# Optimization experiments

Hardware: AMD Instinct MI355X
Metric: run time of the kernel (lower is better)

## Reference

```python
import jax, jax.numpy as jnp
import numpy as np

BETA = 0.9
TH = 1.0
SLOPE = 25.0  # fast-sigmoid surrogate slope (spike_grad_slope)

@jax.custom_vjp
def spike_fn(m):
    # Heaviside on (mem - threshold)
    return (m > 0).astype(m.dtype)

def _spike_fwd(m):
    return spike_fn(m), m

def _spike_bwd(m, g):
    # fast-sigmoid surrogate gradient: 1 / (slope*|m| + 1)^2
    return (g / (SLOPE * jnp.abs(m) + 1.0) ** 2,)

spike_fn.defvjp(_spike_fwd, _spike_bwd)


def setup_inputs() -> dict:
    key = jax.random.key(0)
    k1, k2, k3 = jax.random.split(key, 3)
    T, B, I, H, O = 128, 8192, 2, 256, 2
    x = jax.random.normal(k1, (T, B, I), dtype=jnp.float32)
    # xavier_uniform with gain=1: limit = sqrt(6/(fan_in+fan_out))
    lim1 = float(np.sqrt(6.0 / (I + H)))
    lim2 = float(np.sqrt(6.0 / (H + O)))
    W1 = jax.random.uniform(k2, (H, I), jnp.float32, -lim1, lim1)
    W2 = jax.random.uniform(k3, (O, H), jnp.float32, -lim2, lim2)
    return {"x": x, "W1": W1, "W2": W2}


def reference(x, W1, W2):
    # Precompute all per-step input currents in one GEMM: [T,B,H]
    cur = jnp.einsum('tbi,hi->tbh', x, W1)
    B, H = cur.shape[1], cur.shape[2]
    mem0 = jnp.zeros((B, H), cur.dtype)

    def step(mem, c):
        # snntorch Leaky (reset_mechanism='subtract'):
        # reset based on PREVIOUS mem's spike, then leaky integrate, then fire
        reset = spike_fn(mem - TH)
        mem_new = BETA * mem + c - reset * TH
        spk = spike_fn(mem_new - TH)
        # original code detaches mem between steps (1-step truncated BPTT)
        return jax.lax.stop_gradient(mem_new), spk

    _, spk_rec = jax.lax.scan(step, mem0, cur)  # spk_rec: [T,B,H]
    spk_avg = spk_rec[-10:].mean(0)             # [B,H]
    out = jnp.einsum('bh,oh->bo', spk_avg, W2)  # [B,O]
    return out
```

## Files before the change

### kernel.cpp

```cpp
#include <hip/hip_runtime.h>


#define T_STEPS 128
#define BATCH   8192
#define HID     256
#define TAIL    10
#define RH      8
#define NP      (RH/2)
#define LB      64
#define NWAVE   4
#define HG      8
#define NBG     (BATCH / LB)
#define PF      8

typedef float f32x2 __attribute__((ext_vector_type(2)));

#define PK_MUL(d, a, b) asm("v_pk_mul_f32 %0, %1, %2" : "=v"(d) : "v"(a), "v"(b))
#define PK_ADD(d, a, b) asm("v_pk_add_f32 %0, %1, %2" : "=v"(d) : "v"(a), "v"(b))

__device__ unsigned int bg_done[NBG];

__global__ __launch_bounds__(256) void snn_scan(const float* __restrict__ x,
                                                const float* __restrict__ W1,
                                                const float* __restrict__ W2,
                                                float2* __restrict__ partial,
                                                float2* __restrict__ out) {
    const int tid   = threadIdx.x;
    const int lane  = tid & 63;
    const int wave  = tid >> 6;
    const int bg    = blockIdx.x & (NBG - 1);
    const int hg    = blockIdx.x >> 7;
    const int b     = bg * LB + lane;
    const int hbase = hg * (NWAVE * RH) + wave * RH;

    f32x2 w01[RH];
    const f32x2* w1v = (const f32x2*)W1;
#pragma unroll
    for (int r = 0; r < RH; ++r) w01[r] = w1v[hbase + r];

    const f32x2* xp = (const f32x2*)x;

    f32x2 mem[NP], spkn[NP], cnt[NP];
#pragma unroll
    for (int p = 0; p < NP; ++p) {
        mem[p]  = f32x2{0.0f, 0.0f};
        spkn[p] = f32x2{0.0f, 0.0f};
        cnt[p]  = f32x2{0.0f, 0.0f};
    }

    const f32x2 k09 = {0.9f, 0.9f};

#define LOADX(t) xp[(size_t)(t) * BATCH + b]

#define STEPP(p)                                                      \
    {                                                                 \
        f32x2 te, to, cc, m1, m2;                                     \
        PK_MUL(te, xv, w01[2 * (p)]);                                 \
        PK_MUL(to, xv, w01[2 * (p) + 1]);                             \
        cc.x = __fadd_rn(te.x, te.y);                                 \
        cc.y = __fadd_rn(to.x, to.y);                                 \
        PK_MUL(m1, k09, mem[p]);                                      \
        PK_ADD(m2, m1, cc);                                           \
        PK_ADD(mem[p], m2, spkn[p]);                                  \
        spkn[p].x = (mem[p].x > 1.0f) ? -1.0f : 0.0f;                 \
        spkn[p].y = (mem[p].y > 1.0f) ? -1.0f : 0.0f;                 \
    }

    f32x2 buf[PF];
#pragma unroll
    for (int j = 0; j < PF; ++j) buf[j] = LOADX(j);

    for (int tb = 0; tb < T_STEPS - 2 * PF; tb += PF) {
#pragma unroll
        for (int j = 0; j < PF; ++j) {
            const f32x2 xv = buf[j];
            buf[j] = LOADX(tb + PF + j);
#pragma unroll
            for (int p = 0; p < NP; ++p) STEPP(p)
        }
    }

#pragma unroll
    for (int j = 0; j < PF; ++j) {
        const f32x2 xv = buf[j];
        buf[j] = LOADX(T_STEPS - PF + j);
#pragma unroll
        for (int p = 0; p < NP; ++p) {
            STEPP(p)
            if (j >= PF - 2) PK_ADD(cnt[p], cnt[p], spkn[p]);
        }
    }
#pragma unroll
    for (int j = 0; j < PF; ++j) {
        const f32x2 xv = buf[j];
#pragma unroll
        for (int p = 0; p < NP; ++p) {
            STEPP(p)
            PK_ADD(cnt[p], cnt[p], spkn[p]);
        }
    }
#undef STEPP
#undef LOADX

    float p0 = 0.0f, p1 = 0.0f;
#pragma unroll
    for (int p = 0; p < NP; ++p) {
        const float a0 = cnt[p].x / -10.0f;
        p0 = __fadd_rn(p0, __fmul_rn(a0, W2[hbase + 2 * p]));
        p1 = __fadd_rn(p1, __fmul_rn(a0, W2[HID + hbase + 2 * p]));
        const float a1 = cnt[p].y / -10.0f;
        p0 = __fadd_rn(p0, __fmul_rn(a1, W2[hbase + 2 * p + 1]));
        p1 = __fadd_rn(p1, __fmul_rn(a1, W2[HID + hbase + 2 * p + 1]));
    }

    __shared__ float2 red[NWAVE][LB];
    red[wave][lane] = make_float2(p0, p1);
    __syncthreads();
    if (wave == 0) {
        const float2 a0 = red[0][lane], a1 = red[1][lane];
        const float2 a2 = red[2][lane], a3 = red[3][lane];
        float2 s;
        s.x = __fadd_rn(__fadd_rn(a0.x, a1.x), __fadd_rn(a2.x, a3.x));
        s.y = __fadd_rn(__fadd_rn(a0.y, a1.y), __fadd_rn(a2.y, a3.y));
        partial[(size_t)hg * BATCH + b] = s;

        __threadfence();
        unsigned int old = 0;
        if (lane == 0) old = atomicAdd(&bg_done[bg], 1u);
        old = (unsigned int)__shfl((int)old, 0);

        if (old == HG - 1) {
            __threadfence();
            float sx = 0.0f, sy = 0.0f;
#pragma unroll
            for (int hgi = 0; hgi < HG; ++hgi) {
                const float2 pv = partial[(size_t)hgi * BATCH + b];
                sx = __fadd_rn(sx, pv.x);
                sy = __fadd_rn(sy, pv.y);
            }
            out[b] = make_float2(sx, sy);
            if (lane == 0) bg_done[bg] = 0u;
        }
    }
}

extern "C" void kernel_launch(void* const* d_in, const int* in_sizes, int n_in,
                              void* d_out, int out_size, void* d_ws, size_t ws_size,
                              hipStream_t stream) {
    const float* x  = (const float*)d_in[0];
    const float* W1 = (const float*)d_in[1];
    const float* W2 = (const float*)d_in[2];
    float2* out     = (float2*)d_out;
    float2* partial = (float2*)d_ws;

    snn_scan<<<NBG * HG, 256, 0, stream>>>(x, W1, W2, partial, out);
}
```

Before: 124.0 us.

## Halve hidden units per wave, double waves per block, split final reduction kernel

Each wave now handles 4 hidden units instead of 8, and blocks have 8 waves instead of 4, so the scan has twice as many threads with fewer registers each. The intent is more parallelism and occupancy for the latency-bound recurrence. The W2 projection moves to a shared-memory reduction done by wave 0. The atomic last-block reduction is replaced by a separate reduce kernel, which adds a second launch but removes the atomics and fences. Each thread now repeats the x loads and weight multiplies for half as many hidden units, so total x traffic doubles.

Result: faster. 108.9 us (-12.2%).

```diff
diff --git a/kernel.cpp b/kernel.cpp
--- a/kernel.cpp
+++ b/kernel.cpp
@@ -5,10 +5,10 @@
 #define BATCH   8192
 #define HID     256
 #define TAIL    10
-#define RH      8
+#define RH      4
 #define NP      (RH/2)
 #define LB      64
-#define NWAVE   4
+#define NWAVE   8
 #define HG      8
 #define NBG     (BATCH / LB)
 #define PF      8
@@ -18,13 +18,10 @@
 #define PK_MUL(d, a, b) asm("v_pk_mul_f32 %0, %1, %2" : "=v"(d) : "v"(a), "v"(b))
 #define PK_ADD(d, a, b) asm("v_pk_add_f32 %0, %1, %2" : "=v"(d) : "v"(a), "v"(b))
 
-__device__ unsigned int bg_done[NBG];
-
-__global__ __launch_bounds__(256) void snn_scan(const float* __restrict__ x,
-                                                const float* __restrict__ W1,
-                                                const float* __restrict__ W2,
-                                                float2* __restrict__ partial,
-                                                float2* __restrict__ out) {
+__global__ __launch_bounds__(512, 8) void snn_scan(const float* __restrict__ x,
+                                                   const float* __restrict__ W1,
+                                                   const float* __restrict__ W2,
+                                                   float2* __restrict__ partial) {
     const int tid   = threadIdx.x;
     const int lane  = tid & 63;
     const int wave  = tid >> 6;
@@ -102,46 +99,46 @@
 #undef STEPP
 #undef LOADX
 
-    float p0 = 0.0f, p1 = 0.0f;
+    __shared__ float avgs[NWAVE * RH][LB];
 #pragma unroll
     for (int p = 0; p < NP; ++p) {
-        const float a0 = cnt[p].x / -10.0f;
-        p0 = __fadd_rn(p0, __fmul_rn(a0, W2[hbase + 2 * p]));
-        p1 = __fadd_rn(p1, __fmul_rn(a0, W2[HID + hbase + 2 * p]));
-        const float a1 = cnt[p].y / -10.0f;
-        p0 = __fadd_rn(p0, __fmul_rn(a1, W2[hbase + 2 * p + 1]));
-        p1 = __fadd_rn(p1, __fmul_rn(a1, W2[HID + hbase + 2 * p + 1]));
+        avgs[wave * RH + 2 * p][lane]     = cnt[p].x / -10.0f;
+        avgs[wave * RH + 2 * p + 1][lane] = cnt[p].y / -10.0f;
     }
+    __syncthreads();
 
-    __shared__ float2 red[NWAVE][LB];
-    red[wave][lane] = make_float2(p0, p1);
-    __syncthreads();
     if (wave == 0) {
-        const float2 a0 = red[0][lane], a1 = red[1][lane];
-        const float2 a2 = red[2][lane], a3 = red[3][lane];
+        float c0[4], c1[4];
+#pragma unroll
+        for (int k = 0; k < 4; ++k) {
+            float s0 = 0.0f, s1 = 0.0f;
+#pragma unroll
+            for (int j = 0; j < 8; ++j) {
+                const int hl = 8 * k + j;
+                const float a = avgs[hl][lane];
+                s0 = __fadd_rn(s0, __fmul_rn(a, W2[hg * 32 + hl]));
+                s1 = __fadd_rn(s1, __fmul_rn(a, W2[HID + hg * 32 + hl]));
+            }
+            c0[k] = s0; c1[k] = s1;
+        }
         float2 s;
-        s.x = __fadd_rn(__fadd_rn(a0.x, a1.x), __fadd_rn(a2.x, a3.x));
-        s.y = __fadd_rn(__fadd_rn(a0.y, a1.y), __fadd_rn(a2.y, a3.y));
+        s.x = __fadd_rn(__fadd_rn(c0[0], c0[1]), __fadd_rn(c0[2], c0[3]));
+        s.y = __fadd_rn(__fadd_rn(c1[0], c1[1]), __fadd_rn(c1[2], c1[3]));
         partial[(size_t)hg * BATCH + b] = s;
+    }
+}
 
-        __threadfence();
-        unsigned int old = 0;
-        if (lane == 0) old = atomicAdd(&bg_done[bg], 1u);
-        old = (unsigned int)__shfl((int)old, 0);
-
-        if (old == HG - 1) {
-            __threadfence();
-            float sx = 0.0f, sy = 0.0f;
+__global__ __launch_bounds__(256) void snn_reduce(const float2* __restrict__ partial,
+                                                  float2* __restrict__ out) {
+    const int b = blockIdx.x * 256 + threadIdx.x;
+    float sx = 0.0f, sy = 0.0f;
 #pragma unroll
-            for (int hgi = 0; hgi < HG; ++hgi) {
-                const float2 pv = partial[(size_t)hgi * BATCH + b];
-                sx = __fadd_rn(sx, pv.x);
-                sy = __fadd_rn(sy, pv.y);
-            }
-            out[b] = make_float2(sx, sy);
-            if (lane == 0) bg_done[bg] = 0u;
-        }
+    for (int hg = 0; hg < HG; ++hg) {
+        const float2 p = partial[(size_t)hg * BATCH + b];
+        sx = __fadd_rn(sx, p.x);
+        sy = __fadd_rn(sy, p.y);
     }
+    out[b] = make_float2(sx, sy);
 }
 
 extern "C" void kernel_launch(void* const* d_in, const int* in_sizes, int n_in,
@@ -153,5 +150,6 @@
     float2* out     = (float2*)d_out;
     float2* partial = (float2*)d_ws;
 
-    snn_scan<<<NBG * HG, 256, 0, stream>>>(x, W1, W2, partial, out);
+    snn_scan<<<NBG * HG, 512, 0, stream>>>(x, W1, W2, partial);
+    snn_reduce<<<BATCH / 256, 256, 0, stream>>>(partial, out);
 }
```
